# Kernel tuning notes

Hardware: AMD Instinct MI355X
Metric: run time of the kernel (lower is better)

The kernel has to match this reference:

```python
import jax, jax.numpy as jnp
import numpy as np

NUM_HEADS = 8
KEY_DIM = 64
VALUE_DIM = 64
UPDATE_STEPS_MAX = 3
UPDATE_EPS = 1e-4
LN_EPS = 1e-5


def _layernorm(x, gamma, beta):
    # normalize over last axis (key_dim), per build: shape (..., num_heads, key_dim)
    mu = jnp.mean(x, axis=-1, keepdims=True)
    var = jnp.var(x, axis=-1, keepdims=True)
    return (x - mu) * jax.lax.rsqrt(var + LN_EPS) * gamma + beta


def setup_inputs() -> dict:
    key = jax.random.key(0)
    ks = jax.random.split(key, 8)
    D = 512
    B, S = 8, 1024
    s = 1.0 / np.sqrt(D)
    return {
        "x": jax.random.normal(ks[0], (B, S, D), jnp.float32),
        "Wq": jax.random.normal(ks[1], (D, NUM_HEADS * KEY_DIM), jnp.float32) * s,
        "bq": jnp.zeros((NUM_HEADS * KEY_DIM,), jnp.float32),
        "Wk": jax.random.normal(ks[2], (D, NUM_HEADS * KEY_DIM), jnp.float32) * s,
        "bk": jnp.zeros((NUM_HEADS * KEY_DIM,), jnp.float32),
        "Wv": jax.random.normal(ks[3], (D, NUM_HEADS * VALUE_DIM), jnp.float32) * s,
        "bv": jnp.zeros((NUM_HEADS * VALUE_DIM,), jnp.float32),
        "Wo": jax.random.normal(ks[4], (NUM_HEADS * VALUE_DIM, D), jnp.float32) * s,
        "bo": jnp.zeros((D,), jnp.float32),
        "gamma": jnp.ones((KEY_DIM,), jnp.float32),
        "beta": jnp.zeros((KEY_DIM,), jnp.float32),
    }


def reference(x, Wq, bq, Wk, bk, Wv, bv, Wo, bo, gamma, beta):
    B, S, D = x.shape
    H, dk, dv = NUM_HEADS, KEY_DIM, VALUE_DIM
    # QKV projections -> (B, S, H, d)
    q = (x @ Wq + bq).reshape(B, S, H, dk)
    k = (x @ Wk + bk).reshape(B, S, H, dk)
    v = (x @ Wv + bv).reshape(B, S, H, dv)
    # pattern normalization (LayerNorm over key_dim)
    q = _layernorm(q, gamma, beta)
    k = _layernorm(k, gamma, beta)
    # -> (B, H, S, d)
    q = q.transpose(0, 2, 1, 3)
    k = k.transpose(0, 2, 1, 3)
    v = v.transpose(0, 2, 1, 3)
    scale = jnp.sqrt(jnp.asarray(dk, q.dtype))
    # iterative Hopfield association updates: q <- softmax(qK^T/scale) K
    for _ in range(UPDATE_STEPS_MAX):
        attn = jax.nn.softmax(jnp.einsum("bhqd,bhkd->bhqk", q, k) / scale, axis=-1)
        new_q = jnp.einsum("bhqk,bhkd->bhqd", attn, k)
        diff = jnp.linalg.norm(new_q - q)
        q = jnp.where(diff > UPDATE_EPS, new_q, q)  # eps-gated update
    # final retrieval with values
    attn = jax.nn.softmax(jnp.einsum("bhqd,bhkd->bhqk", q, k) / scale, axis=-1)
    out = jnp.einsum("bhqk,bhkd->bhqd", attn, v)
    out = out.transpose(0, 2, 1, 3).reshape(B, S, H * dv)
    return out @ Wo + bo
```

## Files before the change

### kernel.cpp

```cpp
#include <hip/hip_runtime.h>
#include <stdint.h>


#define DEV static __device__ __forceinline__

typedef __attribute__((ext_vector_type(8))) short short8;
typedef __attribute__((ext_vector_type(8))) __bf16 bf16x8;
typedef __attribute__((ext_vector_type(4))) float f32x4;
typedef __attribute__((ext_vector_type(4))) unsigned int uint4v;

DEV unsigned short f2bf(float f) {
  unsigned int u = __builtin_bit_cast(unsigned int, f);
  u = u + 0x7fffu + ((u >> 16) & 1u);
  return (unsigned short)(u >> 16);
}

DEV unsigned int cvtpk(float lo, float hi) {
  unsigned int r;
  asm("v_cvt_pk_bf16_f32 %0, %1, %2" : "=v"(r) : "v"(lo), "v"(hi));
  return r;
}

DEV f32x4 mfma16(short8 a, short8 b, f32x4 c) {
  return __builtin_amdgcn_mfma_f32_16x16x32_bf16(
      __builtin_bit_cast(bf16x8, a), __builtin_bit_cast(bf16x8, b), c, 0, 0, 0);
}

DEV void gload16(void* lds, const void* g) {
  __builtin_amdgcn_global_load_lds(
      (const __attribute__((address_space(1))) void*)(uintptr_t)g,
      (__attribute__((address_space(3))) void*)(unsigned int)(uintptr_t)lds,
      16, 0, 0);
}

__global__ __launch_bounds__(256)
void xcast_kernel(const float* __restrict__ x, unsigned short* __restrict__ xbf) {
  int i = blockIdx.x * 256 + threadIdx.x;
  float4 v = ((const float4*)x)[i];
  ushort4 o;
  o.x = f2bf(v.x); o.y = f2bf(v.y); o.z = f2bf(v.z); o.w = f2bf(v.w);
  ((ushort4*)xbf)[i] = o;
}

__global__ __launch_bounds__(256)
void wtrans_kernel(const float* __restrict__ Wq, const float* __restrict__ Wk,
                   const float* __restrict__ Wv, const float* __restrict__ Wo,
                   unsigned short* __restrict__ wqkvT, unsigned short* __restrict__ woT) {
  __shared__ float t[64][65];
  int job = blockIdx.x;
  int wsel = job >> 6;
  int tile = job & 63;
  int tr = (tile >> 3) * 64;
  int tc = (tile & 7) * 64;
  const float* W = wsel == 0 ? Wq : wsel == 1 ? Wk : wsel == 2 ? Wv : Wo;
  unsigned short* T = wsel < 3 ? wqkvT + (size_t)wsel * 512 * 512 : woT;
  int lane = threadIdx.x & 63;
  int wv = threadIdx.x >> 6;
  for (int rr = 0; rr < 16; ++rr) {
    int r = wv * 16 + rr;
    t[r][lane] = W[(size_t)(tr + r) * 512 + tc + lane];
  }
  __syncthreads();
  for (int rr = 0; rr < 16; ++rr) {
    int r = wv * 16 + rr;
    T[(size_t)(tc + r) * 512 + tr + lane] = f2bf(t[lane][r]);
  }
}

template <int MODE>
__global__ __launch_bounds__(256, 2)
void gemm_kernel(const unsigned short* __restrict__ A,
                 const unsigned short* __restrict__ WT,
                 const float* __restrict__ b0, const float* __restrict__ b1,
                 const float* __restrict__ b2,
                 const float* __restrict__ gamma, const float* __restrict__ beta,
                 unsigned short* __restrict__ Qo, unsigned short* __restrict__ Ko,
                 unsigned short* __restrict__ Vo, float* __restrict__ Fo) {
  __shared__ __align__(16) unsigned char As[2][16384];
  __shared__ __align__(16) unsigned char Ws[2][16384];

  const int tid = threadIdx.x;
  const int lane = tid & 63;
  const int w = tid >> 6;
  const int l15 = lane & 15;
  const int l4 = lane >> 4;
  const int m0 = blockIdx.x * 128;
  const int by = blockIdx.y;
  const int wm = (w >> 1) * 64;
  const int wn = (w & 1) * 64;

  f32x4 acc[4][4];
#pragma unroll
  for (int mt = 0; mt < 4; ++mt)
#pragma unroll
    for (int nt = 0; nt < 4; ++nt) acc[mt][nt] = (f32x4){0.f, 0.f, 0.f, 0.f};

  auto stage = [&](int i) {
    int buf = i & 1;
    int k0 = i * 64;
#pragma unroll
    for (int it = 0; it < 4; ++it) {
      int idx = it * 256 + tid;
      int row = idx >> 3;
      int sc = ((idx & 7) * 16) ^ ((row & 7) << 4);
      gload16(As[buf] + idx * 16,
              (const unsigned char*)A + ((size_t)(m0 + row) * 512 + k0) * 2 + sc);
      gload16(Ws[buf] + idx * 16,
              (const unsigned char*)WT + ((size_t)(by * 128 + row) * 512 + k0) * 2 + sc);
    }
  };

  stage(0);
  __syncthreads();

  for (int i = 0; i < 8; ++i) {
    int buf = i & 1;
    if (i < 7) stage(i + 1);
    __builtin_amdgcn_s_setprio(1);
#pragma unroll
    for (int kk = 0; kk < 2; ++kk) {
      short8 af[4], bfr[4];
#pragma unroll
      for (int mt = 0; mt < 4; ++mt) {
        int row = wm + mt * 16 + l15;
        int colb = (l4 * 16 + kk * 64) ^ ((row & 7) << 4);
        af[mt] = *(const short8*)(As[buf] + row * 128 + colb);
      }
#pragma unroll
      for (int nt = 0; nt < 4; ++nt) {
        int row = wn + nt * 16 + l15;
        int colb = (l4 * 16 + kk * 64) ^ ((row & 7) << 4);
        bfr[nt] = *(const short8*)(Ws[buf] + row * 128 + colb);
      }
#pragma unroll
      for (int mt = 0; mt < 4; ++mt)
#pragma unroll
        for (int nt = 0; nt < 4; ++nt) acc[mt][nt] = mfma16(af[mt], bfr[nt], acc[mt][nt]);
    }
    __builtin_amdgcn_s_setprio(0);
    __syncthreads();
  }

  const float cs = 1.4426950408889634f / 8.0f;
  const float* bias = (MODE == 1) ? b0 : (by >> 2) == 0 ? b0 : (by >> 2) == 1 ? b1 : b2;
  float bvv[4];
#pragma unroll
  for (int nt = 0; nt < 4; ++nt) bvv[nt] = bias[(by & 3) * 128 + wn + nt * 16 + l15];

  if (MODE == 1) {
#pragma unroll
    for (int mt = 0; mt < 4; ++mt)
#pragma unroll
      for (int r = 0; r < 4; ++r) {
        int gr = m0 + wm + mt * 16 + l4 * 4 + r;
#pragma unroll
        for (int nt = 0; nt < 4; ++nt)
          Fo[(size_t)gr * 512 + (by & 3) * 128 + wn + nt * 16 + l15] =
              acc[mt][nt][r] + bvv[nt];
      }
  } else {
    const int seg = by >> 2;
    const int h = (by & 3) * 2 + (wn >> 6);
    if (seg == 2) {
#pragma unroll
      for (int mt = 0; mt < 4; ++mt)
#pragma unroll
        for (int r = 0; r < 4; ++r) {
          int gr = m0 + wm + mt * 16 + l4 * 4 + r;
          int b = gr >> 10, s = gr & 1023;
          size_t base = ((size_t)(b * 8 + h) << 16) + ((size_t)s << 6);
#pragma unroll
          for (int nt = 0; nt < 4; ++nt)
            Vo[base + nt * 16 + l15] = f2bf(acc[mt][nt][r] + bvv[nt]);
        }
    } else {
      float g4[4], be4[4];
#pragma unroll
      for (int nt = 0; nt < 4; ++nt) {
        g4[nt] = gamma[nt * 16 + l15];
        be4[nt] = beta[nt * 16 + l15];
      }
      unsigned short* dst = seg == 0 ? Qo : Ko;
      const float m = seg == 0 ? cs : 1.0f;
#pragma unroll
      for (int mt = 0; mt < 4; ++mt)
#pragma unroll
        for (int r = 0; r < 4; ++r) {
          float v[4];
#pragma unroll
          for (int nt = 0; nt < 4; ++nt) v[nt] = acc[mt][nt][r] + bvv[nt];
          float s1 = (v[0] + v[1]) + (v[2] + v[3]);
          s1 += __shfl_xor(s1, 1); s1 += __shfl_xor(s1, 2);
          s1 += __shfl_xor(s1, 4); s1 += __shfl_xor(s1, 8);
          float mu = s1 * (1.0f / 64.0f);
          float s2 = v[0]*v[0] + v[1]*v[1] + v[2]*v[2] + v[3]*v[3];
          s2 += __shfl_xor(s2, 1); s2 += __shfl_xor(s2, 2);
          s2 += __shfl_xor(s2, 4); s2 += __shfl_xor(s2, 8);
          float var = s2 * (1.0f / 64.0f) - mu * mu;
          float rs = rsqrtf(var + 1e-5f);
          int gr = m0 + wm + mt * 16 + l4 * 4 + r;
          int b = gr >> 10, s = gr & 1023;
          size_t base = ((size_t)(b * 8 + h) << 16) + ((size_t)s << 6);
#pragma unroll
          for (int nt = 0; nt < 4; ++nt) {
            float y = ((v[nt] - mu) * rs * g4[nt] + be4[nt]) * m;
            dst[base + nt * 16 + l15] = f2bf(y);
          }
        }
    }
  }
}

__global__ __launch_bounds__(256)
void ktrans_kernel(const unsigned short* __restrict__ Kb,
                   const unsigned short* __restrict__ Vb,
                   unsigned short* __restrict__ KTg, unsigned short* __restrict__ VTg) {
  __shared__ unsigned short tile[64][65];
  const int c = blockIdx.x;
  const int bh = blockIdx.y;
  const unsigned short* src = blockIdx.z ? Vb : Kb;
  unsigned short* dst = blockIdx.z ? VTg : KTg;
  const int t = threadIdx.x;
  {
    int j = t >> 2, c16 = (t & 3) * 16;
    const unsigned short* sp = src + ((size_t)bh << 16) + ((size_t)(c * 64 + j) << 6) + c16;
    unsigned short vals[16];
    *(uint4*)(vals) = *(const uint4*)(sp);
    *(uint4*)(vals + 8) = *(const uint4*)(sp + 8);
#pragma unroll
    for (int i = 0; i < 16; ++i) tile[j][c16 + i] = vals[i];
  }
  __syncthreads();
  {
    int d = t >> 2, k16 = (t & 3) * 16;
    unsigned short ov[16];
#pragma unroll
    for (int i = 0; i < 16; ++i) {
      int kp = k16 + i;
      int hi = kp >> 5, tt = kp & 31, l4p = tt >> 3, ii = tt & 7;
      int g = (hi * 2 + (ii >> 2)) * 16 + l4p * 4 + (ii & 3);
      ov[i] = tile[g][d];
    }
    unsigned short* dp = dst + ((size_t)bh << 16) + ((size_t)d << 10) + c * 64 + k16;
    *(uint4*)(dp) = *(uint4*)(ov);
    *(uint4*)(dp + 8) = *(uint4*)(ov + 8);
  }
}

__global__ __launch_bounds__(512, 4)
void attn_kernel(const unsigned short* __restrict__ Qb,
                 const unsigned short* __restrict__ Kb,
                 const unsigned short* __restrict__ KTg,
                 const unsigned short* __restrict__ VTg,
                 unsigned short* __restrict__ Ob) {
  __shared__ __align__(16) unsigned char Kc[2][8192];
  __shared__ __align__(16) unsigned char Tc[2][8192];
  __shared__ __align__(16) unsigned char Qw[8][2048];

  const int tid = threadIdx.x;
  const int lane = tid & 63;
  const int w = tid >> 6;
  const int l15 = lane & 15;
  const int l4 = lane >> 4;
  const int bh = blockIdx.y;
  const int q0 = blockIdx.x * 128 + w * 16;
  const size_t kvbase = (size_t)bh << 16;
  const float cs = 1.4426950408889634f / 8.0f;

  const int srow = tid >> 3;
  const int scolb = ((tid & 7) * 16) ^ ((srow & 7) << 4);
  const unsigned char* kSrc = (const unsigned char*)(Kb + kvbase) + (size_t)srow * 128 + scolb;
  const unsigned char* tKSrc = (const unsigned char*)(KTg + kvbase) + (size_t)srow * 2048 + scolb;
  const unsigned char* tVSrc = (const unsigned char*)(VTg + kvbase) + (size_t)srow * 2048 + scolb;

  auto stage = [&](int t) {
    int c = t & 15, buf = t & 1;
    gload16(Kc[buf] + tid * 16, kSrc + (size_t)c * 8192);
    const unsigned char* ts = (t >= 48) ? tVSrc : tKSrc;
    gload16(Tc[buf] + tid * 16, ts + c * 128);
  };

  stage(0);
  __syncthreads();

  short8 qf0, qf1;
  {
    const unsigned short* qp = Qb + kvbase + ((size_t)(q0 + l15) << 6) + l4 * 8;
    qf0 = *(const short8*)qp;
    qf1 = *(const short8*)(qp + 32);
  }

  f32x4 acc[4];
#pragma unroll
  for (int dt = 0; dt < 4; ++dt) acc[dt] = (f32x4){0.f, 0.f, 0.f, 0.f};
  float lsum = 0.f;

  for (int t = 0; t < 64; ++t) {
    const int buf = t & 1;
    if (t < 63) stage(t + 1);

    f32x4 sc[4];
    __builtin_amdgcn_s_setprio(1);
#pragma unroll
    for (int kt = 0; kt < 4; ++kt) {
      int row = kt * 16 + l15;
      int sw = (row & 7) << 4;
      short8 kf0 = *(const short8*)(Kc[buf] + row * 128 + ((l4 * 16) ^ sw));
      short8 kf1 = *(const short8*)(Kc[buf] + row * 128 + ((64 + l4 * 16) ^ sw));
      f32x4 s = (f32x4){0.f, 0.f, 0.f, 0.f};
      s = mfma16(kf0, qf0, s);
      s = mfma16(kf1, qf1, s);
      sc[kt] = s;
    }
    __builtin_amdgcn_s_setprio(0);

    unsigned int pku[8];
#pragma unroll
    for (int kt = 0; kt < 4; ++kt) {
      float p0 = exp2f(sc[kt][0]);
      float p1 = exp2f(sc[kt][1]);
      float p2 = exp2f(sc[kt][2]);
      float p3 = exp2f(sc[kt][3]);
      lsum += (p0 + p1) + (p2 + p3);
      pku[kt * 2] = cvtpk(p0, p1);
      pku[kt * 2 + 1] = cvtpk(p2, p3);
    }
    short8 pa0 = __builtin_bit_cast(short8, (uint4v){pku[0], pku[1], pku[2], pku[3]});
    short8 pa1 = __builtin_bit_cast(short8, (uint4v){pku[4], pku[5], pku[6], pku[7]});

    __builtin_amdgcn_s_setprio(1);
#pragma unroll
    for (int dt = 0; dt < 4; ++dt) {
      int row = dt * 16 + l15;
      int sw = (row & 7) << 4;
      short8 tf0 = *(const short8*)(Tc[buf] + row * 128 + ((l4 * 16) ^ sw));
      short8 tf1 = *(const short8*)(Tc[buf] + row * 128 + ((64 + l4 * 16) ^ sw));
      acc[dt] = mfma16(pa0, tf0, acc[dt]);
      acc[dt] = mfma16(pa1, tf1, acc[dt]);
    }
    __builtin_amdgcn_s_setprio(0);

    if ((t & 15) == 15) {
      float l = lsum;
      l += __shfl_xor(l, 16);
      l += __shfl_xor(l, 32);
      float inv = 1.0f / l;
      float invr[4];
#pragma unroll
      for (int r = 0; r < 4; ++r) invr[r] = __shfl(inv, l4 * 4 + r);
      if (t < 48) {
#pragma unroll
        for (int dt = 0; dt < 4; ++dt)
#pragma unroll
          for (int r = 0; r < 4; ++r) {
            int row = l4 * 4 + r;
            int colb = (2 * (dt * 16 + l15)) ^ ((row & 7) << 4);
            *(unsigned short*)(Qw[w] + row * 128 + colb) =
                f2bf(acc[dt][r] * invr[r] * cs);
          }
        {
          int sw = (l15 & 7) << 4;
          qf0 = *(const short8*)(Qw[w] + l15 * 128 + ((l4 * 16) ^ sw));
          qf1 = *(const short8*)(Qw[w] + l15 * 128 + ((64 + l4 * 16) ^ sw));
        }
#pragma unroll
        for (int dt = 0; dt < 4; ++dt) acc[dt] = (f32x4){0.f, 0.f, 0.f, 0.f};
        lsum = 0.f;
      } else {
        const int b = bh >> 3, h = bh & 7;
#pragma unroll
        for (int dt = 0; dt < 4; ++dt)
#pragma unroll
          for (int r = 0; r < 4; ++r) {
            int s = q0 + l4 * 4 + r;
            Ob[((size_t)(b * 1024 + s) << 9) + h * 64 + dt * 16 + l15] =
                f2bf(acc[dt][r] * invr[r]);
          }
      }
    }
    __syncthreads();
  }
}

extern "C" void kernel_launch(void* const* d_in, const int* in_sizes, int n_in,
                              void* d_out, int out_size, void* d_ws, size_t ws_size,
                              hipStream_t stream) {
  const float* x  = (const float*)d_in[0];
  const float* Wq = (const float*)d_in[1];
  const float* bq = (const float*)d_in[2];
  const float* Wk = (const float*)d_in[3];
  const float* bk = (const float*)d_in[4];
  const float* Wv = (const float*)d_in[5];
  const float* bv = (const float*)d_in[6];
  const float* Wo = (const float*)d_in[7];
  const float* bo = (const float*)d_in[8];
  const float* gamma = (const float*)d_in[9];
  const float* beta  = (const float*)d_in[10];
  (void)in_sizes; (void)n_in; (void)out_size; (void)ws_size;

  char* ws = (char*)d_ws;
  size_t off = 0;
  auto alloc = [&](size_t bytes) {
    char* p = ws + off;
    off += (bytes + 255) & ~(size_t)255;
    return p;
  };
  unsigned short* xbf   = (unsigned short*)alloc(8192ull * 512 * 2);
  unsigned short* wqkvT = (unsigned short*)alloc(1536ull * 512 * 2);
  unsigned short* woT   = (unsigned short*)alloc(512ull * 512 * 2);
  unsigned short* Qbf   = (unsigned short*)alloc(64ull * 1024 * 64 * 2);
  unsigned short* Kbf   = (unsigned short*)alloc(64ull * 1024 * 64 * 2);
  unsigned short* Vbf   = (unsigned short*)alloc(64ull * 1024 * 64 * 2);
  unsigned short* KTg   = (unsigned short*)alloc(64ull * 1024 * 64 * 2);
  unsigned short* VTg   = (unsigned short*)alloc(64ull * 1024 * 64 * 2);
  unsigned short* Obf   = (unsigned short*)alloc(8192ull * 512 * 2);

  xcast_kernel<<<4096, 256, 0, stream>>>(x, xbf);
  wtrans_kernel<<<256, 256, 0, stream>>>(Wq, Wk, Wv, Wo, wqkvT, woT);

  gemm_kernel<0><<<dim3(64, 12), 256, 0, stream>>>(
      xbf, wqkvT, bq, bk, bv, gamma, beta, Qbf, Kbf, Vbf, nullptr);

  ktrans_kernel<<<dim3(16, 64, 2), 256, 0, stream>>>(Kbf, Vbf, KTg, VTg);

  attn_kernel<<<dim3(8, 64), 512, 0, stream>>>(Qbf, Kbf, KTg, VTg, Obf);

  gemm_kernel<1><<<dim3(64, 4), 256, 0, stream>>>(
      Obf, woT, bo, nullptr, nullptr, nullptr, nullptr,
      nullptr, nullptr, nullptr, (float*)d_out);
}
```

Before: 232.0 us.

## Switch Hopfield attention to 32x32 MFMA tiles with register-resident query updates

```diff
diff --git a/kernel.cpp b/kernel.cpp
--- a/kernel.cpp
+++ b/kernel.cpp
@@ -7,6 +7,7 @@
 typedef __attribute__((ext_vector_type(8))) short short8;
 typedef __attribute__((ext_vector_type(8))) __bf16 bf16x8;
 typedef __attribute__((ext_vector_type(4))) float f32x4;
+typedef __attribute__((ext_vector_type(16))) float f32x16;
 typedef __attribute__((ext_vector_type(4))) unsigned int uint4v;
 
 DEV unsigned short f2bf(float f) {
@@ -24,6 +25,18 @@
 DEV f32x4 mfma16(short8 a, short8 b, f32x4 c) {
   return __builtin_amdgcn_mfma_f32_16x16x32_bf16(
       __builtin_bit_cast(bf16x8, a), __builtin_bit_cast(bf16x8, b), c, 0, 0, 0);
+}
+
+DEV f32x16 mfma32(short8 a, short8 b, f32x16 c) {
+  return __builtin_amdgcn_mfma_f32_32x32x16_bf16(
+      __builtin_bit_cast(bf16x8, a), __builtin_bit_cast(bf16x8, b), c, 0, 0, 0);
+}
+
+DEV f32x16 zero16() {
+  f32x16 z;
+#pragma unroll
+  for (int i = 0; i < 16; ++i) z[i] = 0.f;
+  return z;
 }
 
 DEV void gload16(void* lds, const void* g) {
@@ -237,9 +250,10 @@
 #pragma unroll
     for (int i = 0; i < 16; ++i) {
       int kp = k16 + i;
-      int hi = kp >> 5, tt = kp & 31, l4p = tt >> 3, ii = tt & 7;
-      int g = (hi * 2 + (ii >> 2)) * 16 + l4p * 4 + (ii & 3);
-      ov[i] = tile[g][d];
+      int g = kp >> 5, r5 = kp & 31;
+      int c16 = r5 >> 4, h = (r5 >> 3) & 1, ii = r5 & 7;
+      int phys = g * 32 + c16 * 16 + 8 * (ii >> 2) + 4 * h + (ii & 3);
+      ov[i] = tile[phys][d];
     }
     unsigned short* dp = dst + ((size_t)bh << 16) + ((size_t)d << 10) + c * 64 + k16;
     *(uint4*)(dp) = *(uint4*)(ov);
@@ -247,7 +261,7 @@
   }
 }
 
-__global__ __launch_bounds__(512, 4)
+__global__ __launch_bounds__(256, 2)
 void attn_kernel(const unsigned short* __restrict__ Qb,
                  const unsigned short* __restrict__ Kb,
                  const unsigned short* __restrict__ KTg,
@@ -255,130 +269,179 @@
                  unsigned short* __restrict__ Ob) {
   __shared__ __align__(16) unsigned char Kc[2][8192];
   __shared__ __align__(16) unsigned char Tc[2][8192];
-  __shared__ __align__(16) unsigned char Qw[8][2048];
 
   const int tid = threadIdx.x;
   const int lane = tid & 63;
   const int w = tid >> 6;
-  const int l15 = lane & 15;
-  const int l4 = lane >> 4;
-  const int bh = blockIdx.y;
-  const int q0 = blockIdx.x * 128 + w * 16;
-  const size_t kvbase = (size_t)bh << 16;
+  const int l31 = lane & 31;
+  const int hi = lane >> 5;
+  const int bi = blockIdx.x;
+  const int xcd = bi & 7, wnd = bi >> 3;
+  const int bh = xcd * 8 + (wnd & 7);
+  const int qt = wnd >> 3;
+  const int q0 = qt * 128 + w * 32;
+  const size_t kvb = (size_t)bh << 17;
   const float cs = 1.4426950408889634f / 8.0f;
 
-  const int srow = tid >> 3;
-  const int scolb = ((tid & 7) * 16) ^ ((srow & 7) << 4);
-  const unsigned char* kSrc = (const unsigned char*)(Kb + kvbase) + (size_t)srow * 128 + scolb;
-  const unsigned char* tKSrc = (const unsigned char*)(KTg + kvbase) + (size_t)srow * 2048 + scolb;
-  const unsigned char* tVSrc = (const unsigned char*)(VTg + kvbase) + (size_t)srow * 2048 + scolb;
+  int sOffK[2], sOffT[2];
+#pragma unroll
+  for (int it = 0; it < 2; ++it) {
+    int idx = it * 256 + tid;
+    int row = idx >> 3;
+    int colb = ((idx & 7) * 16) ^ ((row & 7) << 4);
+    sOffK[it] = row * 128 + colb;
+    sOffT[it] = row * 2048 + colb;
+  }
+  const unsigned char* kS = (const unsigned char*)Kb + kvb;
+  const unsigned char* tKS = (const unsigned char*)KTg + kvb;
+  const unsigned char* tVS = (const unsigned char*)VTg + kvb;
 
   auto stage = [&](int t) {
     int c = t & 15, buf = t & 1;
-    gload16(Kc[buf] + tid * 16, kSrc + (size_t)c * 8192);
-    const unsigned char* ts = (t >= 48) ? tVSrc : tKSrc;
-    gload16(Tc[buf] + tid * 16, ts + c * 128);
+    const unsigned char* ts = (t >= 48) ? tVS : tKS;
+#pragma unroll
+    for (int it = 0; it < 2; ++it) {
+      int idx = it * 256 + tid;
+      gload16(Kc[buf] + idx * 16, kS + (size_t)c * 8192 + sOffK[it]);
+      gload16(Tc[buf] + idx * 16, ts + (size_t)c * 128 + sOffT[it]);
+    }
   };
 
   stage(0);
+
+  short8 qf[4];
+  {
+    const unsigned char* qp =
+        (const unsigned char*)Qb + kvb + ((size_t)(q0 + l31) << 7) + hi * 16;
+    qf[0] = *(const short8*)(qp);
+    qf[1] = *(const short8*)(qp + 32);
+    qf[2] = *(const short8*)(qp + 64);
+    qf[3] = *(const short8*)(qp + 96);
+  }
+
+  f32x16 acc0 = zero16(), acc1 = zero16();
+  float lsum = 0.f;
+  const int sw = (l31 & 7) << 4;
+  const int hb = hi * 16;
+  const int rowA = l31 * 128;
+
+  auto compute = [&](int buf) {
+    const unsigned char* KB = Kc[buf];
+    const unsigned char* TB = Tc[buf];
+    short8 kfa[4], kfb[4];
+#pragma unroll
+    for (int s = 0; s < 4; ++s) {
+      int cb = (32 * s + hb) ^ sw;
+      kfa[s] = *(const short8*)(KB + rowA + cb);
+      kfb[s] = *(const short8*)(KB + 4096 + rowA + cb);
+    }
+    f32x16 s0 = zero16(), s1 = zero16();
+    __builtin_amdgcn_s_setprio(1);
+#pragma unroll
+    for (int s = 0; s < 4; ++s) {
+      s0 = mfma32(kfa[s], qf[s], s0);
+      s1 = mfma32(kfb[s], qf[s], s1);
+    }
+    __builtin_amdgcn_s_setprio(0);
+    unsigned int u0[8], u1[8];
+#pragma unroll
+    for (int r = 0; r < 16; r += 2) {
+      float pA = exp2f(s0[r]), pB = exp2f(s0[r + 1]);
+      lsum += pA + pB;
+      u0[r >> 1] = cvtpk(pA, pB);
+    }
+#pragma unroll
+    for (int r = 0; r < 16; r += 2) {
+      float pA = exp2f(s1[r]), pB = exp2f(s1[r + 1]);
+      lsum += pA + pB;
+      u1[r >> 1] = cvtpk(pA, pB);
+    }
+    short8 p00 = __builtin_bit_cast(short8, (uint4v){u0[0], u0[1], u0[2], u0[3]});
+    short8 p01 = __builtin_bit_cast(short8, (uint4v){u0[4], u0[5], u0[6], u0[7]});
+    short8 p10 = __builtin_bit_cast(short8, (uint4v){u1[0], u1[1], u1[2], u1[3]});
+    short8 p11 = __builtin_bit_cast(short8, (uint4v){u1[4], u1[5], u1[6], u1[7]});
+    short8 t0, t1;
+    __builtin_amdgcn_s_setprio(1);
+    t0 = *(const short8*)(TB + rowA + ((0 + hb) ^ sw));
+    t1 = *(const short8*)(TB + 4096 + rowA + ((0 + hb) ^ sw));
+    acc0 = mfma32(t0, p00, acc0);
+    acc1 = mfma32(t1, p00, acc1);
+    t0 = *(const short8*)(TB + rowA + ((32 + hb) ^ sw));
+    t1 = *(const short8*)(TB + 4096 + rowA + ((32 + hb) ^ sw));
+    acc0 = mfma32(t0, p01, acc0);
+    acc1 = mfma32(t1, p01, acc1);
+    t0 = *(const short8*)(TB + rowA + ((64 + hb) ^ sw));
+    t1 = *(const short8*)(TB + 4096 + rowA + ((64 + hb) ^ sw));
+    acc0 = mfma32(t0, p10, acc0);
+    acc1 = mfma32(t1, p10, acc1);
+    t0 = *(const short8*)(TB + rowA + ((96 + hb) ^ sw));
+    t1 = *(const short8*)(TB + 4096 + rowA + ((96 + hb) ^ sw));
+    acc0 = mfma32(t0, p11, acc0);
+    acc1 = mfma32(t1, p11, acc1);
+    __builtin_amdgcn_s_setprio(0);
+  };
+
   __syncthreads();
 
-  short8 qf0, qf1;
-  {
-    const unsigned short* qp = Qb + kvbase + ((size_t)(q0 + l15) << 6) + l4 * 8;
-    qf0 = *(const short8*)qp;
-    qf1 = *(const short8*)(qp + 32);
-  }
-
-  f32x4 acc[4];
-#pragma unroll
-  for (int dt = 0; dt < 4; ++dt) acc[dt] = (f32x4){0.f, 0.f, 0.f, 0.f};
-  float lsum = 0.f;
-
-  for (int t = 0; t < 64; ++t) {
-    const int buf = t & 1;
-    if (t < 63) stage(t + 1);
-
-    f32x4 sc[4];
-    __builtin_amdgcn_s_setprio(1);
-#pragma unroll
-    for (int kt = 0; kt < 4; ++kt) {
-      int row = kt * 16 + l15;
-      int sw = (row & 7) << 4;
-      short8 kf0 = *(const short8*)(Kc[buf] + row * 128 + ((l4 * 16) ^ sw));
-      short8 kf1 = *(const short8*)(Kc[buf] + row * 128 + ((64 + l4 * 16) ^ sw));
-      f32x4 s = (f32x4){0.f, 0.f, 0.f, 0.f};
-      s = mfma16(kf0, qf0, s);
-      s = mfma16(kf1, qf1, s);
-      sc[kt] = s;
-    }
-    __builtin_amdgcn_s_setprio(0);
-
-    unsigned int pku[8];
-#pragma unroll
-    for (int kt = 0; kt < 4; ++kt) {
-      float p0 = exp2f(sc[kt][0]);
-      float p1 = exp2f(sc[kt][1]);
-      float p2 = exp2f(sc[kt][2]);
-      float p3 = exp2f(sc[kt][3]);
-      lsum += (p0 + p1) + (p2 + p3);
-      pku[kt * 2] = cvtpk(p0, p1);
-      pku[kt * 2 + 1] = cvtpk(p2, p3);
-    }
-    short8 pa0 = __builtin_bit_cast(short8, (uint4v){pku[0], pku[1], pku[2], pku[3]});
-    short8 pa1 = __builtin_bit_cast(short8, (uint4v){pku[4], pku[5], pku[6], pku[7]});
-
-    __builtin_amdgcn_s_setprio(1);
-#pragma unroll
-    for (int dt = 0; dt < 4; ++dt) {
-      int row = dt * 16 + l15;
-      int sw = (row & 7) << 4;
-      short8 tf0 = *(const short8*)(Tc[buf] + row * 128 + ((l4 * 16) ^ sw));
-      short8 tf1 = *(const short8*)(Tc[buf] + row * 128 + ((64 + l4 * 16) ^ sw));
-      acc[dt] = mfma16(pa0, tf0, acc[dt]);
-      acc[dt] = mfma16(pa1, tf1, acc[dt]);
-    }
-    __builtin_amdgcn_s_setprio(0);
-
-    if ((t & 15) == 15) {
-      float l = lsum;
-      l += __shfl_xor(l, 16);
-      l += __shfl_xor(l, 32);
-      float inv = 1.0f / l;
-      float invr[4];
-#pragma unroll
-      for (int r = 0; r < 4; ++r) invr[r] = __shfl(inv, l4 * 4 + r);
-      if (t < 48) {
-#pragma unroll
-        for (int dt = 0; dt < 4; ++dt)
-#pragma unroll
-          for (int r = 0; r < 4; ++r) {
-            int row = l4 * 4 + r;
-            int colb = (2 * (dt * 16 + l15)) ^ ((row & 7) << 4);
-            *(unsigned short*)(Qw[w] + row * 128 + colb) =
-                f2bf(acc[dt][r] * invr[r] * cs);
-          }
-        {
-          int sw = (l15 & 7) << 4;
-          qf0 = *(const short8*)(Qw[w] + l15 * 128 + ((l4 * 16) ^ sw));
-          qf1 = *(const short8*)(Qw[w] + l15 * 128 + ((64 + l4 * 16) ^ sw));
+  for (int p = 0; p < 4; ++p) {
+    for (int c2 = 0; c2 < 16; c2 += 2) {
+      {
+        int t = p * 16 + c2;
+        if (t < 63) stage(t + 1);
+        compute(0);
+        __syncthreads();
+      }
+      {
+        int t = p * 16 + c2 + 1;
+        if (t < 63) stage(t + 1);
+        compute(1);
+        __syncthreads();
+      }
+    }
+    lsum += __shfl_xor(lsum, 32);
+    if (p < 3) {
+      float f = cs / lsum;
+#pragma unroll
+      for (int s = 0; s < 4; ++s) {
+        const f32x16& A = (s >> 1) ? acc1 : acc0;
+        const int base = 8 * (s & 1);
+        float a0 = A[base] * f, a1 = A[base + 1] * f;
+        float a2 = A[base + 2] * f, a3 = A[base + 3] * f;
+        float b0 = A[base + 4] * f, b1 = A[base + 5] * f;
+        float b2 = A[base + 6] * f, b3 = A[base + 7] * f;
+        float s0_ = hi ? a0 : b0, s1_ = hi ? a1 : b1;
+        float s2_ = hi ? a2 : b2, s3_ = hi ? a3 : b3;
+        float r0 = __shfl_xor(s0_, 32), r1 = __shfl_xor(s1_, 32);
+        float r2 = __shfl_xor(s2_, 32), r3 = __shfl_xor(s3_, 32);
+        float e0 = hi ? r0 : a0, e1 = hi ? r1 : a1;
+        float e2 = hi ? r2 : a2, e3 = hi ? r3 : a3;
+        float e4 = hi ? b0 : r0, e5 = hi ? b1 : r1;
+        float e6 = hi ? b2 : r2, e7 = hi ? b3 : r3;
+        qf[s] = __builtin_bit_cast(
+            short8, (uint4v){cvtpk(e0, e1), cvtpk(e2, e3), cvtpk(e4, e5), cvtpk(e6, e7)});
+      }
+      acc0 = zero16();
+      acc1 = zero16();
+      lsum = 0.f;
+    } else {
+      float inv = 1.0f / lsum;
+      const int b = bh >> 3, h = bh & 7;
+      const int qg = q0 + l31;
+      unsigned short* orow = Ob + ((size_t)(b * 1024 + qg) << 9) + h * 64;
+#pragma unroll
+      for (int dt = 0; dt < 2; ++dt) {
+        const f32x16& A = dt ? acc1 : acc0;
+#pragma unroll
+        for (int rq = 0; rq < 4; ++rq) {
+          ushort4 o;
+          o.x = f2bf(A[4 * rq + 0] * inv);
+          o.y = f2bf(A[4 * rq + 1] * inv);
+          o.z = f2bf(A[4 * rq + 2] * inv);
+          o.w = f2bf(A[4 * rq + 3] * inv);
+          *(ushort4*)(orow + dt * 32 + 8 * rq + 4 * hi) = o;
         }
-#pragma unroll
-        for (int dt = 0; dt < 4; ++dt) acc[dt] = (f32x4){0.f, 0.f, 0.f, 0.f};
-        lsum = 0.f;
-      } else {
-        const int b = bh >> 3, h = bh & 7;
-#pragma unroll
-        for (int dt = 0; dt < 4; ++dt)
-#pragma unroll
-          for (int r = 0; r < 4; ++r) {
-            int s = q0 + l4 * 4 + r;
-            Ob[((size_t)(b * 1024 + s) << 9) + h * 64 + dt * 16 + l15] =
-                f2bf(acc[dt][r] * invr[r]);
-          }
-      }
-    }
-    __syncthreads();
+      }
+    }
   }
 }
 
@@ -423,7 +486,7 @@
 
   ktrans_kernel<<<dim3(16, 64, 2), 256, 0, stream>>>(Kbf, Vbf, KTg, VTg);
 
-  attn_kernel<<<dim3(8, 64), 512, 0, stream>>>(Qbf, Kbf, KTg, VTg, Obf);
+  attn_kernel<<<512, 256, 0, stream>>>(Qbf, Kbf, KTg, VTg, Obf);
 
   gemm_kernel<1><<<dim3(64, 4), 256, 0, stream>>>(
       Obf, woT, bo, nullptr, nullptr, nullptr, nullptr,
```

Result: no change. 231.5 us (-0.2%).
